# Performance work log

Hardware: AMD Instinct MI355X
Metric: run time of the kernel (lower is better)

## Reference

```python
import jax, jax.numpy as jnp
import numpy as np

N_NODES = 50000
N_EDGES = 800000
IN_DIM = 32
HID = 64
OUT_DIM = 4
HEADS = 4
LAYERS = 3
N_GRAPHS = 50
NEG_SLOPE = 0.2
BN_EPS = 1e-5


def setup_inputs() -> dict:
    key = jax.random.key(0)
    ks = jax.random.split(key, 20)
    x = jax.random.normal(ks[0], (N_NODES, IN_DIM), dtype=jnp.float32)
    edge_index = jax.random.randint(ks[1], (2, N_EDGES), 0, N_NODES, dtype=jnp.int64)
    batch = jnp.sort(jax.random.randint(ks[2], (N_NODES,), 0, N_GRAPHS, dtype=jnp.int64))
    s = 0.05
    inp = {
        "x": x,
        "edge_index": edge_index,
        "batch": batch,
        "in_W": jax.random.normal(ks[3], (IN_DIM, HID), jnp.float32) * s,
        "in_b": jnp.zeros((HID,), jnp.float32),
        "gat_W": jax.random.normal(ks[4], (LAYERS, HID, HEADS * HID), jnp.float32) * s,
        "att_src": jax.random.normal(ks[5], (LAYERS, HEADS, HID), jnp.float32) * s,
        "att_dst": jax.random.normal(ks[6], (LAYERS, HEADS, HID), jnp.float32) * s,
        "gat_b": jnp.zeros((LAYERS, HID), jnp.float32),
        "bn_g": jnp.ones((LAYERS, HID), jnp.float32),
        "bn_b": jnp.zeros((LAYERS, HID), jnp.float32),
        "bn_m": jnp.zeros((LAYERS, HID), jnp.float32),
        "bn_v": jnp.ones((LAYERS, HID), jnp.float32),
        "fc1_W": jax.random.normal(ks[7], (HID, HID), jnp.float32) * s,
        "fc1_b": jnp.zeros((HID,), jnp.float32),
        "fc2_W": jax.random.normal(ks[8], (HID, OUT_DIM), jnp.float32) * s,
        "fc2_b": jnp.zeros((OUT_DIM,), jnp.float32),
    }
    return inp


def _gat_layer(x, src, dst, W, a_src, a_dst, b):
    # x: [N, HID]; src/dst: [E'] (self-loops included)
    N = x.shape[0]
    xt = (x @ W).reshape(N, HEADS, HID)           # [N, H, C]
    sc_src = jnp.einsum("nhc,hc->nh", xt, a_src)  # [N, H]
    sc_dst = jnp.einsum("nhc,hc->nh", xt, a_dst)
    e = jax.nn.leaky_relu(sc_src[src] + sc_dst[dst], NEG_SLOPE)  # [E, H]
    # segment softmax over incoming edges of each dst node
    emax = jax.ops.segment_max(e, dst, num_segments=N)
    ex = jnp.exp(e - emax[dst])
    denom = jax.ops.segment_sum(ex, dst, num_segments=N)
    alpha = ex / (denom[dst] + 1e-16)             # [E, H]
    msg = xt[src] * alpha[:, :, None]             # [E, H, C]
    out = jax.ops.segment_sum(msg, dst, num_segments=N)  # [N, H, C]
    return out.mean(axis=1) + b                   # head-average (concat=False)


def reference(x, edge_index, batch, in_W, in_b, gat_W, att_src, att_dst, gat_b,
              bn_g, bn_b, bn_m, bn_v, fc1_W, fc1_b, fc2_W, fc2_b):
    N = x.shape[0]
    loops = jnp.arange(N, dtype=edge_index.dtype)
    src = jnp.concatenate([edge_index[0], loops])
    dst = jnp.concatenate([edge_index[1], loops])

    h = x @ in_W + in_b  # dropout: eval mode (identity)
    for i in range(LAYERS):
        identity = h
        h = _gat_layer(h, src, dst, gat_W[i], att_src[i], att_dst[i], gat_b[i])
        # BatchNorm1d in eval mode (running stats)
        h = (h - bn_m[i]) * jax.lax.rsqrt(bn_v[i] + BN_EPS) * bn_g[i] + bn_b[i]
        h = jax.nn.relu(h)
        h = h + identity

    # global mean pool over graphs
    sums = jax.ops.segment_sum(h, batch, num_segments=N_GRAPHS)
    cnt = jax.ops.segment_sum(jnp.ones((N,), h.dtype), batch, num_segments=N_GRAPHS)
    g = sums / jnp.maximum(cnt, 1.0)[:, None]     # [N_GRAPHS, HID]

    g = jax.nn.relu(g @ fc1_W + fc1_b)
    return g @ fc2_W + fc2_b                      # [N_GRAPHS, OUT_DIM]
```

## Files before the change

### kernel.cpp

```cpp
#include <hip/hip_runtime.h>
#include <hip/hip_fp16.h>
#include <math.h>

#define HID 64
#define HEADS 4
#define HC 256
#define IN_DIM 32
#define NEG 0.2f
#define BN_EPS 1e-5f
#define CAP 64

__device__ __forceinline__ int ld_idx(const int* __restrict__ p, int i, int f64) {
    return f64 ? p[(size_t)2 * i] : p[i];
}

__global__ void k_init(const int* __restrict__ ei, int* __restrict__ flag,
                       int* __restrict__ deg, float* __restrict__ gsum,
                       int N, int NG) {
    int i = blockIdx.x * blockDim.x + threadIdx.x;
    if (i == 0) {
        int z = 1;
#pragma unroll
        for (int k = 1; k < 64; k += 2) z &= (ei[k] == 0);
        *flag = z;
    }
    if (i < N) deg[i] = 0;
    if (i < NG) gsum[i] = 0.f;
}

template <typename IT>
__global__ void k_build(const int* __restrict__ ei, const int* __restrict__ flagp,
                        int* __restrict__ deg, IT* __restrict__ src_pad, int E) {
    int e = blockIdx.x * blockDim.x + threadIdx.x;
    if (e >= E) return;
    const int f = *flagp;
    int s = ld_idx(ei, e, f);
    int d = ld_idx(ei, E + e, f);
    int pos = atomicAdd(&deg[d], 1);
    if (pos < CAP) src_pad[(size_t)d * CAP + pos] = (IT)s;
}

__global__ void k_wtilde(const float* __restrict__ gat_W, const float* __restrict__ asrc,
                         const float* __restrict__ adst, float* __restrict__ wts,
                         float* __restrict__ wtd) {
    int l = blockIdx.x;
    int t = threadIdx.x;
    int hh = t >> 6, k = t & 63;
    const float* W = gat_W + (size_t)l * HID * HC + (size_t)k * HC + hh * HID;
    const float* as = asrc + (size_t)l * HEADS * HID + hh * HID;
    const float* ad = adst + (size_t)l * HEADS * HID + hh * HID;
    float s1 = 0.f, s2 = 0.f;
#pragma unroll
    for (int c = 0; c < HID; ++c) { s1 += W[c] * as[c]; s2 += W[c] * ad[c]; }
    wts[l * HC + hh * HID + k] = s1;
    wtd[l * HC + hh * HID + k] = s2;
}

__global__ __launch_bounds__(256) void k_input(
        const float* __restrict__ x, const float* __restrict__ W,
        const float* __restrict__ b, const float* __restrict__ wts0,
        const float* __restrict__ wtd0, float* __restrict__ h,
        __half* __restrict__ h16, float* __restrict__ ssrc,
        float* __restrict__ sdst, int N) {
    int w = threadIdx.x >> 6, lane = threadIdx.x & 63;
    int n = blockIdx.x * 4 + w;
    if (n >= N) return;
    float xv = x[(size_t)n * IN_DIM + (lane & 31)];
    float acc = b[lane];
#pragma unroll
    for (int k = 0; k < IN_DIM; ++k)
        acc += __shfl(xv, k, 64) * W[k * HID + lane];
    h[(size_t)n * HID + lane] = acc;
    h16[(size_t)n * HID + lane] = __float2half(acc);
    float p0 = acc * wts0[0 * HID + lane];
    float p1 = acc * wts0[1 * HID + lane];
    float p2 = acc * wts0[2 * HID + lane];
    float p3 = acc * wts0[3 * HID + lane];
    float q0 = acc * wtd0[0 * HID + lane];
    float q1 = acc * wtd0[1 * HID + lane];
    float q2 = acc * wtd0[2 * HID + lane];
    float q3 = acc * wtd0[3 * HID + lane];
#pragma unroll
    for (int m = 32; m >= 1; m >>= 1) {
        p0 += __shfl_xor(p0, m, 64); p1 += __shfl_xor(p1, m, 64);
        p2 += __shfl_xor(p2, m, 64); p3 += __shfl_xor(p3, m, 64);
        q0 += __shfl_xor(q0, m, 64); q1 += __shfl_xor(q1, m, 64);
        q2 += __shfl_xor(q2, m, 64); q3 += __shfl_xor(q3, m, 64);
    }
    if (lane == 0) {
        *(float4*)(ssrc + (size_t)n * HEADS) = make_float4(p0, p1, p2, p3);
        *(float4*)(sdst + (size_t)n * HEADS) = make_float4(q0, q1, q2, q3);
    }
}

template <typename IT>
__global__ __launch_bounds__(256) void k_gather(
        const int* __restrict__ deg, const IT* __restrict__ src_pad,
        const float* __restrict__ ssrc, const float* __restrict__ sdst,
        const __half* __restrict__ h16, __half* __restrict__ agg, int N) {
    int d = blockIdx.x * 4 + (threadIdx.x >> 6);
    if (d >= N) return;
    const int lane = threadIdx.x & 63;
    const int g = lane >> 4, l16 = lane & 15;
    const int dg = min(deg[d], CAP);
    const int se = (int)src_pad[(size_t)d * CAP + lane];
    const float4 sdd = *(const float4*)(sdst + (size_t)d * HEADS);
    float den0 = 0.f, den1 = 0.f, den2 = 0.f, den3 = 0.f;
    float a00=0.f,a01=0.f,a02=0.f,a03=0.f, a10=0.f,a11=0.f,a12=0.f,a13=0.f;
    float a20=0.f,a21=0.f,a22=0.f,a23=0.f, a30=0.f,a31=0.f,a32=0.f,a33=0.f;
    {
        float4 ssd = *(const float4*)(ssrc + (size_t)d * HEADS);
        uint2 hu = *(const uint2*)(h16 + (size_t)d * HID + l16 * 4);
        float2 f01 = __half22float2(*(__half2*)&hu.x);
        float2 f23 = __half22float2(*(__half2*)&hu.y);
        if (g == 0) {
            float v0 = ssd.x + sdd.x; v0 = v0 > 0.f ? v0 : NEG * v0;
            float v1 = ssd.y + sdd.y; v1 = v1 > 0.f ? v1 : NEG * v1;
            float v2 = ssd.z + sdd.z; v2 = v2 > 0.f ? v2 : NEG * v2;
            float v3 = ssd.w + sdd.w; v3 = v3 > 0.f ? v3 : NEG * v3;
            float e0 = __expf(v0), e1 = __expf(v1), e2 = __expf(v2), e3 = __expf(v3);
            den0 = e0; den1 = e1; den2 = e2; den3 = e3;
            a00 = e0*f01.x; a01 = e0*f01.y; a02 = e0*f23.x; a03 = e0*f23.y;
            a10 = e1*f01.x; a11 = e1*f01.y; a12 = e1*f23.x; a13 = e1*f23.y;
            a20 = e2*f01.x; a21 = e2*f01.y; a22 = e2*f23.x; a23 = e2*f23.y;
            a30 = e3*f01.x; a31 = e3*f01.y; a32 = e3*f23.x; a33 = e3*f23.y;
        }
    }
    for (int b = 0; b < dg; b += 4) {
        int idx = b + g;
        bool valid = idx < dg;
        int s = __shfl(se, idx, 64);
        s = valid ? s : d;
        float4 ss = *(const float4*)(ssrc + (size_t)s * HEADS);
        uint2 hu = *(const uint2*)(h16 + (size_t)s * HID + l16 * 4);
        float u0 = ss.x + sdd.x; u0 = u0 > 0.f ? u0 : NEG * u0;
        float u1 = ss.y + sdd.y; u1 = u1 > 0.f ? u1 : NEG * u1;
        float u2 = ss.z + sdd.z; u2 = u2 > 0.f ? u2 : NEG * u2;
        float u3 = ss.w + sdd.w; u3 = u3 > 0.f ? u3 : NEG * u3;
        float e0 = valid ? __expf(u0) : 0.f;
        float e1 = valid ? __expf(u1) : 0.f;
        float e2 = valid ? __expf(u2) : 0.f;
        float e3 = valid ? __expf(u3) : 0.f;
        float2 f01 = __half22float2(*(__half2*)&hu.x);
        float2 f23 = __half22float2(*(__half2*)&hu.y);
        den0 += e0; den1 += e1; den2 += e2; den3 += e3;
        a00 += e0*f01.x; a01 += e0*f01.y; a02 += e0*f23.x; a03 += e0*f23.y;
        a10 += e1*f01.x; a11 += e1*f01.y; a12 += e1*f23.x; a13 += e1*f23.y;
        a20 += e2*f01.x; a21 += e2*f01.y; a22 += e2*f23.x; a23 += e2*f23.y;
        a30 += e3*f01.x; a31 += e3*f01.y; a32 += e3*f23.x; a33 += e3*f23.y;
    }
#define FOLD(v) { v += __shfl_xor(v, 16, 64); v += __shfl_xor(v, 32, 64); }
    FOLD(den0) FOLD(den1) FOLD(den2) FOLD(den3)
    FOLD(a00) FOLD(a01) FOLD(a02) FOLD(a03)
    FOLD(a10) FOLD(a11) FOLD(a12) FOLD(a13)
    FOLD(a20) FOLD(a21) FOLD(a22) FOLD(a23)
    FOLD(a30) FOLD(a31) FOLD(a32) FOLD(a33)
#undef FOLD
    float iv, o0, o1, o2, o3;
    if (g == 0)      { iv = 0.25f / den0; o0 = a00; o1 = a01; o2 = a02; o3 = a03; }
    else if (g == 1) { iv = 0.25f / den1; o0 = a10; o1 = a11; o2 = a12; o3 = a13; }
    else if (g == 2) { iv = 0.25f / den2; o0 = a20; o1 = a21; o2 = a22; o3 = a23; }
    else             { iv = 0.25f / den3; o0 = a30; o1 = a31; o2 = a32; o3 = a33; }
    __half2 q01 = __floats2half2_rn(o0 * iv, o1 * iv);
    __half2 q23 = __floats2half2_rn(o2 * iv, o3 * iv);
    uint2 st;
    st.x = *(unsigned int*)&q01;
    st.y = *(unsigned int*)&q23;
    *(uint2*)(agg + ((size_t)d * HC + g * HID + l16 * 4)) = st;
}

#define PWB 16
__global__ __launch_bounds__(256) void k_postW(
        const __half* __restrict__ agg, const float* __restrict__ W,
        const float* __restrict__ gb, const float* __restrict__ bg,
        const float* __restrict__ bb, const float* __restrict__ bm,
        const float* __restrict__ bv, const float* __restrict__ wtsn,
        const float* __restrict__ wtdn, float* __restrict__ h,
        __half* __restrict__ h16, float* __restrict__ ssrc,
        float* __restrict__ sdst, int N) {
    __shared__ float sm[PWB * HC];
    const int t = threadIdx.x;
    const int n0 = blockIdx.x * PWB;
    {
        int j = t >> 4, c0 = (t & 15) * 16;
        float* dst = &sm[j * HC + c0];
        if (n0 + j < N) {
            const __half* src = agg + ((size_t)(n0 + j) * HC + c0);
            uint4 u0 = *(const uint4*)(src);
            uint4 u1 = *(const uint4*)(src + 8);
            const __half2* p0 = (const __half2*)&u0;
            const __half2* p1 = (const __half2*)&u1;
#pragma unroll
            for (int i = 0; i < 4; ++i) {
                float2 f = __half22float2(p0[i]);
                dst[2 * i] = f.x; dst[2 * i + 1] = f.y;
            }
#pragma unroll
            for (int i = 0; i < 4; ++i) {
                float2 f = __half22float2(p1[i]);
                dst[8 + 2 * i] = f.x; dst[8 + 2 * i + 1] = f.y;
            }
        } else {
#pragma unroll
            for (int i = 0; i < 16; ++i) dst[i] = 0.f;
        }
    }
    float wreg[HID];
#pragma unroll
    for (int k = 0; k < HID; ++k) wreg[k] = W[k * HC + t];
    __syncthreads();
    const int hh = t >> 6;
    float p[PWB];
#pragma unroll
    for (int j = 0; j < PWB; ++j) {
        const float* row = &sm[j * HC + hh * HID];
        float s = 0.f;
#pragma unroll
        for (int kk = 0; kk < HID / 4; ++kk) {
            float4 a = *(const float4*)(row + kk * 4);
            s += a.x * wreg[4 * kk + 0] + a.y * wreg[4 * kk + 1]
               + a.z * wreg[4 * kk + 2] + a.w * wreg[4 * kk + 3];
        }
        p[j] = s;
    }
    __syncthreads();
#pragma unroll
    for (int j = 0; j < PWB; ++j) sm[j * HC + t] = p[j];
    __syncthreads();
    {
        int j = t >> 4, c0 = (t & 15) * 4;
        int n = n0 + j;
        if (n < N) {
            float4 s0 = *(const float4*)&sm[j * HC + c0];
            float4 s1 = *(const float4*)&sm[j * HC + 64 + c0];
            float4 s2 = *(const float4*)&sm[j * HC + 128 + c0];
            float4 s3 = *(const float4*)&sm[j * HC + 192 + c0];
            float* hrow = h + (size_t)n * HID;
            float4 r = *(const float4*)(hrow + c0);
            float4 gb4 = *(const float4*)(gb + c0);
            float4 bg4 = *(const float4*)(bg + c0);
            float4 bb4 = *(const float4*)(bb + c0);
            float4 bm4 = *(const float4*)(bm + c0);
            float4 bv4 = *(const float4*)(bv + c0);
            float4 o;
            {
                float v = s0.x + s1.x + s2.x + s3.x + gb4.x;
                v = (v - bm4.x) * rsqrtf(bv4.x + BN_EPS) * bg4.x + bb4.x;
                o.x = fmaxf(v, 0.f) + r.x;
            }
            {
                float v = s0.y + s1.y + s2.y + s3.y + gb4.y;
                v = (v - bm4.y) * rsqrtf(bv4.y + BN_EPS) * bg4.y + bb4.y;
                o.y = fmaxf(v, 0.f) + r.y;
            }
            {
                float v = s0.z + s1.z + s2.z + s3.z + gb4.z;
                v = (v - bm4.z) * rsqrtf(bv4.z + BN_EPS) * bg4.z + bb4.z;
                o.z = fmaxf(v, 0.f) + r.z;
            }
            {
                float v = s0.w + s1.w + s2.w + s3.w + gb4.w;
                v = (v - bm4.w) * rsqrtf(bv4.w + BN_EPS) * bg4.w + bb4.w;
                o.w = fmaxf(v, 0.f) + r.w;
            }
            *(float4*)(hrow + c0) = o;
            __half2 ha = __floats2half2_rn(o.x, o.y);
            __half2 hb = __floats2half2_rn(o.z, o.w);
            uint2 hu;
            hu.x = *(unsigned int*)&ha;
            hu.y = *(unsigned int*)&hb;
            *(uint2*)(h16 + (size_t)n * HID + c0) = hu;
            if (wtsn) {
                float ps0 = 0.f, ps1 = 0.f, ps2 = 0.f, ps3 = 0.f;
                float pd0 = 0.f, pd1 = 0.f, pd2 = 0.f, pd3 = 0.f;
#pragma unroll
                for (int i = 0; i < 4; ++i) {
                    int c = c0 + i;
                    float ov = i == 0 ? o.x : i == 1 ? o.y : i == 2 ? o.z : o.w;
                    ps0 += ov * wtsn[0 * HID + c]; ps1 += ov * wtsn[1 * HID + c];
                    ps2 += ov * wtsn[2 * HID + c]; ps3 += ov * wtsn[3 * HID + c];
                    pd0 += ov * wtdn[0 * HID + c]; pd1 += ov * wtdn[1 * HID + c];
                    pd2 += ov * wtdn[2 * HID + c]; pd3 += ov * wtdn[3 * HID + c];
                }
#pragma unroll
                for (int m = 8; m >= 1; m >>= 1) {
                    ps0 += __shfl_xor(ps0, m, 64); ps1 += __shfl_xor(ps1, m, 64);
                    ps2 += __shfl_xor(ps2, m, 64); ps3 += __shfl_xor(ps3, m, 64);
                    pd0 += __shfl_xor(pd0, m, 64); pd1 += __shfl_xor(pd1, m, 64);
                    pd2 += __shfl_xor(pd2, m, 64); pd3 += __shfl_xor(pd3, m, 64);
                }
                if ((t & 15) == 0) {
                    *(float4*)(ssrc + (size_t)n * HEADS) = make_float4(ps0, ps1, ps2, ps3);
                    *(float4*)(sdst + (size_t)n * HEADS) = make_float4(pd0, pd1, pd2, pd3);
                }
            }
        }
    }
}

#define NPBK 64
__global__ void k_pool_sum(const float* __restrict__ h, const int* __restrict__ batch,
                           const int* __restrict__ flagp, float* __restrict__ gsum, int N) {
    const int f = *flagp;
    int c = threadIdx.x;
    int n0 = blockIdx.x * NPBK;
    int n1 = min(n0 + NPBK, N);
    if (n0 >= N) return;
    int cur = ld_idx(batch, n0, f);
    float s = 0.f;
    for (int n = n0; n < n1; ++n) {
        int g = ld_idx(batch, n, f);
        if (g != cur) {
            atomicAdd(&gsum[cur * HID + c], s);
            s = 0.f;
            cur = g;
        }
        s += h[(size_t)n * HID + c];
    }
    atomicAdd(&gsum[cur * HID + c], s);
}

__device__ __forceinline__ int lower_bound_i(const int* __restrict__ a, int n, int v, int f) {
    int lo = 0, hi = n;
    while (lo < hi) {
        int mid = (lo + hi) >> 1;
        if (ld_idx(a, mid, f) < v) lo = mid + 1; else hi = mid;
    }
    return lo;
}

__global__ void k_mlp(const float* __restrict__ gsum, const int* __restrict__ batch,
                      const int* __restrict__ flagp, int N,
                      const float* __restrict__ W1, const float* __restrict__ b1,
                      const float* __restrict__ W2, const float* __restrict__ b2,
                      float* __restrict__ out, int OUTD) {
    int gg = blockIdx.x, c = threadIdx.x;
    const int f = *flagp;
    int lo = lower_bound_i(batch, N, gg, f);
    int hi = lower_bound_i(batch, N, gg + 1, f);
    float cnt = (float)(hi - lo);
    __shared__ float gs[HID];
    __shared__ float s1[HID];
    gs[c] = gsum[gg * HID + c] / fmaxf(cnt, 1.f);
    __syncthreads();
    float acc = b1[c];
#pragma unroll
    for (int k = 0; k < HID; ++k) acc += gs[k] * W1[k * HID + c];
    s1[c] = fmaxf(acc, 0.f);
    __syncthreads();
    if (c < OUTD) {
        float o = b2[c];
#pragma unroll
        for (int k = 0; k < HID; ++k) o += s1[k] * W2[k * OUTD + c];
        out[gg * OUTD + c] = o;
    }
}

extern "C" void kernel_launch(void* const* d_in, const int* in_sizes, int n_in,
                              void* d_out, int out_size, void* d_ws, size_t ws_size,
                              hipStream_t stream) {
    const float* x       = (const float*)d_in[0];
    const int*   ei_raw  = (const int*)d_in[1];
    const int*   b_raw   = (const int*)d_in[2];
    const float* in_W    = (const float*)d_in[3];
    const float* in_b    = (const float*)d_in[4];
    const float* gat_W   = (const float*)d_in[5];
    const float* att_src = (const float*)d_in[6];
    const float* att_dst = (const float*)d_in[7];
    const float* gat_b   = (const float*)d_in[8];
    const float* bn_g    = (const float*)d_in[9];
    const float* bn_b    = (const float*)d_in[10];
    const float* bn_m    = (const float*)d_in[11];
    const float* bn_v    = (const float*)d_in[12];
    const float* fc1_W   = (const float*)d_in[13];
    const float* fc1_b   = (const float*)d_in[14];
    const float* fc2_W   = (const float*)d_in[15];
    const float* fc2_b   = (const float*)d_in[16];

    const int N = in_sizes[2];
    const int E = in_sizes[1] / 2;
    const int OUTD = 4;
    const int G = out_size / OUTD;

    float*  h    = (float*)d_ws;
    __half* h16  = (__half*)(h + (size_t)N * HID);
    __half* agg  = h16 + (size_t)N * HID;
    float*  ssrc = (float*)(agg + (size_t)N * HC);
    float*  sdst = ssrc + (size_t)N * HEADS;
    float*  wts  = sdst + (size_t)N * HEADS;
    float*  wtd  = wts + 3 * HC;
    float*  gsum = wtd + 3 * HC;
    int*    deg  = (int*)(gsum + (size_t)G * HID);
    unsigned short* src_pad = (unsigned short*)(deg + N);
    int*    flag = (int*)(src_pad + (size_t)N * CAP);

    k_init<<<(max(N, G * HID) + 255) / 256, 256, 0, stream>>>(
        ei_raw, flag, deg, gsum, N, G * HID);
    k_build<unsigned short><<<(E + 255) / 256, 256, 0, stream>>>(
        ei_raw, flag, deg, src_pad, E);
    k_wtilde<<<3, 256, 0, stream>>>(gat_W, att_src, att_dst, wts, wtd);
    k_input<<<(N + 3) / 4, 256, 0, stream>>>(x, in_W, in_b, wts, wtd, h, h16,
                                             ssrc, sdst, N);

    for (int l = 0; l < 3; ++l) {
        k_gather<unsigned short><<<(N + 3) / 4, 256, 0, stream>>>(
            deg, src_pad, ssrc, sdst, h16, agg, N);
        const float* wtsn = (l < 2) ? (wts + (l + 1) * HC) : nullptr;
        const float* wtdn = (l < 2) ? (wtd + (l + 1) * HC) : nullptr;
        k_postW<<<(N + PWB - 1) / PWB, 256, 0, stream>>>(
            agg, gat_W + (size_t)l * HID * HC,
            gat_b + (size_t)l * HID, bn_g + (size_t)l * HID, bn_b + (size_t)l * HID,
            bn_m + (size_t)l * HID, bn_v + (size_t)l * HID,
            wtsn, wtdn, h, h16, ssrc, sdst, N);
    }

    k_pool_sum<<<(N + NPBK - 1) / NPBK, HID, 0, stream>>>(h, b_raw, flag, gsum, N);
    k_mlp<<<G, HID, 0, stream>>>(gsum, b_raw, flag, N, fc1_W, fc1_b, fc2_W, fc2_b,
                                 (float*)d_out, OUTD);
}
```

Before: 375.1 us.

## Use MFMA for post-aggregation GEMM and bucket edges before CSR build

Replaces the scalar-FMA per-node projection in k_postW with fp16 MFMA 16x16x32 instructions, using a pre-transposed fp16 copy of the GAT weights and 64 rows per block. It also splits adjacency construction into two passes. Edges are first partitioned into 256-node destination buckets, reusing the agg buffer as scratch, and then each bucket is expanded into padded source lists, so the per-node degree atomics stay local. Weights are rounded to fp16, which reduces precision. Edge order within each node's list can now differ, and any bucket that overflows its capacity silently drops edges.

```diff
diff --git a/kernel.cpp b/kernel.cpp
--- a/kernel.cpp
+++ b/kernel.cpp
@@ -10,13 +10,17 @@
 #define BN_EPS 1e-5f
 #define CAP 64
 
+typedef _Float16 f16;
+typedef _Float16 f16x8 __attribute__((ext_vector_type(8)));
+typedef float f32x4 __attribute__((ext_vector_type(4)));
+
 __device__ __forceinline__ int ld_idx(const int* __restrict__ p, int i, int f64) {
     return f64 ? p[(size_t)2 * i] : p[i];
 }
 
 __global__ void k_init(const int* __restrict__ ei, int* __restrict__ flag,
-                       int* __restrict__ deg, float* __restrict__ gsum,
-                       int N, int NG) {
+                       int* __restrict__ deg, int* __restrict__ cursor,
+                       float* __restrict__ gsum, int N, int NG) {
     int i = blockIdx.x * blockDim.x + threadIdx.x;
     if (i == 0) {
         int z = 1;
@@ -25,19 +29,36 @@
         *flag = z;
     }
     if (i < N) deg[i] = 0;
+    if (i < 256) cursor[i] = 0;
     if (i < NG) gsum[i] = 0.f;
 }
 
-template <typename IT>
-__global__ void k_build(const int* __restrict__ ei, const int* __restrict__ flagp,
-                        int* __restrict__ deg, IT* __restrict__ src_pad, int E) {
+__global__ void k_part(const int* __restrict__ ei, const int* __restrict__ flagp,
+                       int* __restrict__ cursor, unsigned int* __restrict__ edge_tmp,
+                       int E, int capb) {
     int e = blockIdx.x * blockDim.x + threadIdx.x;
     if (e >= E) return;
     const int f = *flagp;
-    int s = ld_idx(ei, e, f);
-    int d = ld_idx(ei, E + e, f);
-    int pos = atomicAdd(&deg[d], 1);
-    if (pos < CAP) src_pad[(size_t)d * CAP + pos] = (IT)s;
+    unsigned int s = (unsigned int)ld_idx(ei, e, f);
+    unsigned int d = (unsigned int)ld_idx(ei, E + e, f);
+    int b = d >> 8;
+    int pos = atomicAdd(&cursor[b], 1);
+    if (pos < capb)
+        edge_tmp[(size_t)b * capb + pos] = ((d & 255u) << 16) | s;
+}
+
+__global__ void k_bucket(const unsigned int* __restrict__ edge_tmp,
+                         const int* __restrict__ cursor, int* __restrict__ deg,
+                         unsigned short* __restrict__ src_pad, int capb, int N) {
+    int b = blockIdx.x;
+    int cnt = min(cursor[b], capb);
+    for (int i = threadIdx.x; i < cnt; i += blockDim.x) {
+        unsigned int rec = edge_tmp[(size_t)b * capb + i];
+        int d = (b << 8) + (int)(rec >> 16);
+        int s = (int)(rec & 0xffffu);
+        int pos = atomicAdd(&deg[d], 1);
+        if (pos < CAP) src_pad[(size_t)d * CAP + pos] = (unsigned short)s;
+    }
 }
 
 __global__ void k_wtilde(const float* __restrict__ gat_W, const float* __restrict__ asrc,
@@ -54,6 +75,17 @@
     for (int c = 0; c < HID; ++c) { s1 += W[c] * as[c]; s2 += W[c] * ad[c]; }
     wts[l * HC + hh * HID + k] = s1;
     wtd[l * HC + hh * HID + k] = s2;
+}
+
+__global__ void k_prepB(const float* __restrict__ gat_W, __half* __restrict__ BT) {
+    int l = blockIdx.x;
+    int t = threadIdx.x;
+    int c = t & 63, jg = t >> 6;
+    const float* W = gat_W + (size_t)l * HID * HC;
+    __half* o = BT + (size_t)l * HID * HC + (size_t)c * HC + jg * 64;
+#pragma unroll
+    for (int jj = 0; jj < 64; ++jj)
+        o[jj] = __float2half(W[(size_t)jj * HC + jg * 64 + c]);
 }
 
 __global__ __launch_bounds__(256) void k_input(
@@ -93,9 +125,8 @@
     }
 }
 
-template <typename IT>
 __global__ __launch_bounds__(256) void k_gather(
-        const int* __restrict__ deg, const IT* __restrict__ src_pad,
+        const int* __restrict__ deg, const unsigned short* __restrict__ src_pad,
         const float* __restrict__ ssrc, const float* __restrict__ sdst,
         const __half* __restrict__ h16, __half* __restrict__ agg, int N) {
     int d = blockIdx.x * 4 + (threadIdx.x >> 6);
@@ -169,127 +200,108 @@
     *(uint2*)(agg + ((size_t)d * HC + g * HID + l16 * 4)) = st;
 }
 
-#define PWB 16
 __global__ __launch_bounds__(256) void k_postW(
-        const __half* __restrict__ agg, const float* __restrict__ W,
+        const __half* __restrict__ agg, const __half* __restrict__ BT,
         const float* __restrict__ gb, const float* __restrict__ bg,
         const float* __restrict__ bb, const float* __restrict__ bm,
         const float* __restrict__ bv, const float* __restrict__ wtsn,
         const float* __restrict__ wtdn, float* __restrict__ h,
         __half* __restrict__ h16, float* __restrict__ ssrc,
         float* __restrict__ sdst, int N) {
-    __shared__ float sm[PWB * HC];
+    __shared__ float lds[64][68];
     const int t = threadIdx.x;
-    const int n0 = blockIdx.x * PWB;
-    {
-        int j = t >> 4, c0 = (t & 15) * 16;
-        float* dst = &sm[j * HC + c0];
-        if (n0 + j < N) {
-            const __half* src = agg + ((size_t)(n0 + j) * HC + c0);
-            uint4 u0 = *(const uint4*)(src);
-            uint4 u1 = *(const uint4*)(src + 8);
-            const __half2* p0 = (const __half2*)&u0;
-            const __half2* p1 = (const __half2*)&u1;
-#pragma unroll
-            for (int i = 0; i < 4; ++i) {
-                float2 f = __half22float2(p0[i]);
-                dst[2 * i] = f.x; dst[2 * i + 1] = f.y;
-            }
-#pragma unroll
-            for (int i = 0; i < 4; ++i) {
-                float2 f = __half22float2(p1[i]);
-                dst[8 + 2 * i] = f.x; dst[8 + 2 * i + 1] = f.y;
-            }
-        } else {
-#pragma unroll
-            for (int i = 0; i < 16; ++i) dst[i] = 0.f;
-        }
-    }
-    float wreg[HID];
-#pragma unroll
-    for (int k = 0; k < HID; ++k) wreg[k] = W[k * HC + t];
-    __syncthreads();
-    const int hh = t >> 6;
-    float p[PWB];
-#pragma unroll
-    for (int j = 0; j < PWB; ++j) {
-        const float* row = &sm[j * HC + hh * HID];
-        float s = 0.f;
-#pragma unroll
-        for (int kk = 0; kk < HID / 4; ++kk) {
-            float4 a = *(const float4*)(row + kk * 4);
-            s += a.x * wreg[4 * kk + 0] + a.y * wreg[4 * kk + 1]
-               + a.z * wreg[4 * kk + 2] + a.w * wreg[4 * kk + 3];
-        }
-        p[j] = s;
-    }
-    __syncthreads();
-#pragma unroll
-    for (int j = 0; j < PWB; ++j) sm[j * HC + t] = p[j];
+    const int w = t >> 6, l = t & 63;
+    const int l16 = l & 15, lk = l >> 4;
+    const f16* BTf = (const f16*)BT;
+    const f16* af = (const f16*)agg;
+    f16x8 bf[8][4];
+#pragma unroll
+    for (int ks = 0; ks < 8; ++ks)
+#pragma unroll
+        for (int nt = 0; nt < 4; ++nt)
+            bf[ks][nt] = *(const f16x8*)(BTf + (size_t)(nt * 16 + l16) * HC + ks * 32 + lk * 8);
+    int row = blockIdx.x * 64 + w * 16 + l16;
+    int rowc = min(row, N - 1);
+    f32x4 acc[4];
+#pragma unroll
+    for (int nt = 0; nt < 4; ++nt) acc[nt] = (f32x4){0.f, 0.f, 0.f, 0.f};
+#pragma unroll
+    for (int ks = 0; ks < 8; ++ks) {
+        f16x8 a = *(const f16x8*)(af + (size_t)rowc * HC + ks * 32 + lk * 8);
+#pragma unroll
+        for (int nt = 0; nt < 4; ++nt)
+            acc[nt] = __builtin_amdgcn_mfma_f32_16x16x32_f16(a, bf[ks][nt], acc[nt], 0, 0, 0);
+    }
+#pragma unroll
+    for (int nt = 0; nt < 4; ++nt)
+#pragma unroll
+        for (int r = 0; r < 4; ++r)
+            lds[w * 16 + lk * 4 + r][nt * 16 + l16] = acc[nt][r];
     __syncthreads();
     {
-        int j = t >> 4, c0 = (t & 15) * 4;
-        int n = n0 + j;
+        int j = t >> 2, q = t & 3;
+        int n = blockIdx.x * 64 + j;
         if (n < N) {
-            float4 s0 = *(const float4*)&sm[j * HC + c0];
-            float4 s1 = *(const float4*)&sm[j * HC + 64 + c0];
-            float4 s2 = *(const float4*)&sm[j * HC + 128 + c0];
-            float4 s3 = *(const float4*)&sm[j * HC + 192 + c0];
+            int c0 = q * 16;
+            float o[16];
             float* hrow = h + (size_t)n * HID;
-            float4 r = *(const float4*)(hrow + c0);
-            float4 gb4 = *(const float4*)(gb + c0);
-            float4 bg4 = *(const float4*)(bg + c0);
-            float4 bb4 = *(const float4*)(bb + c0);
-            float4 bm4 = *(const float4*)(bm + c0);
-            float4 bv4 = *(const float4*)(bv + c0);
-            float4 o;
-            {
-                float v = s0.x + s1.x + s2.x + s3.x + gb4.x;
-                v = (v - bm4.x) * rsqrtf(bv4.x + BN_EPS) * bg4.x + bb4.x;
-                o.x = fmaxf(v, 0.f) + r.x;
+#pragma unroll
+            for (int i4 = 0; i4 < 4; ++i4) {
+                int c = c0 + i4 * 4;
+                float4 sv = *(const float4*)&lds[j][c];
+                float4 r4 = *(const float4*)(hrow + c);
+                float4 gb4 = *(const float4*)(gb + c);
+                float4 bg4 = *(const float4*)(bg + c);
+                float4 bb4 = *(const float4*)(bb + c);
+                float4 bm4 = *(const float4*)(bm + c);
+                float4 bv4 = *(const float4*)(bv + c);
+                float4 ov;
+                float v;
+                v = sv.x + gb4.x; v = (v - bm4.x) * rsqrtf(bv4.x + BN_EPS) * bg4.x + bb4.x;
+                ov.x = fmaxf(v, 0.f) + r4.x;
+                v = sv.y + gb4.y; v = (v - bm4.y) * rsqrtf(bv4.y + BN_EPS) * bg4.y + bb4.y;
+                ov.y = fmaxf(v, 0.f) + r4.y;
+                v = sv.z + gb4.z; v = (v - bm4.z) * rsqrtf(bv4.z + BN_EPS) * bg4.z + bb4.z;
+                ov.z = fmaxf(v, 0.f) + r4.z;
+                v = sv.w + gb4.w; v = (v - bm4.w) * rsqrtf(bv4.w + BN_EPS) * bg4.w + bb4.w;
+                ov.w = fmaxf(v, 0.f) + r4.w;
+                *(float4*)(hrow + c) = ov;
+                o[i4 * 4 + 0] = ov.x; o[i4 * 4 + 1] = ov.y;
+                o[i4 * 4 + 2] = ov.z; o[i4 * 4 + 3] = ov.w;
             }
             {
-                float v = s0.y + s1.y + s2.y + s3.y + gb4.y;
-                v = (v - bm4.y) * rsqrtf(bv4.y + BN_EPS) * bg4.y + bb4.y;
-                o.y = fmaxf(v, 0.f) + r.y;
+                __half2 hp[8];
+#pragma unroll
+                for (int i = 0; i < 8; ++i)
+                    hp[i] = __floats2half2_rn(o[2 * i], o[2 * i + 1]);
+                uint4 u0, u1;
+                u0.x = *(unsigned*)&hp[0]; u0.y = *(unsigned*)&hp[1];
+                u0.z = *(unsigned*)&hp[2]; u0.w = *(unsigned*)&hp[3];
+                u1.x = *(unsigned*)&hp[4]; u1.y = *(unsigned*)&hp[5];
+                u1.z = *(unsigned*)&hp[6]; u1.w = *(unsigned*)&hp[7];
+                *(uint4*)(h16 + (size_t)n * HID + c0) = u0;
+                *(uint4*)(h16 + (size_t)n * HID + c0 + 8) = u1;
             }
-            {
-                float v = s0.z + s1.z + s2.z + s3.z + gb4.z;
-                v = (v - bm4.z) * rsqrtf(bv4.z + BN_EPS) * bg4.z + bb4.z;
-                o.z = fmaxf(v, 0.f) + r.z;
-            }
-            {
-                float v = s0.w + s1.w + s2.w + s3.w + gb4.w;
-                v = (v - bm4.w) * rsqrtf(bv4.w + BN_EPS) * bg4.w + bb4.w;
-                o.w = fmaxf(v, 0.f) + r.w;
-            }
-            *(float4*)(hrow + c0) = o;
-            __half2 ha = __floats2half2_rn(o.x, o.y);
-            __half2 hb = __floats2half2_rn(o.z, o.w);
-            uint2 hu;
-            hu.x = *(unsigned int*)&ha;
-            hu.y = *(unsigned int*)&hb;
-            *(uint2*)(h16 + (size_t)n * HID + c0) = hu;
             if (wtsn) {
                 float ps0 = 0.f, ps1 = 0.f, ps2 = 0.f, ps3 = 0.f;
                 float pd0 = 0.f, pd1 = 0.f, pd2 = 0.f, pd3 = 0.f;
 #pragma unroll
-                for (int i = 0; i < 4; ++i) {
+                for (int i = 0; i < 16; ++i) {
                     int c = c0 + i;
-                    float ov = i == 0 ? o.x : i == 1 ? o.y : i == 2 ? o.z : o.w;
+                    float ov = o[i];
                     ps0 += ov * wtsn[0 * HID + c]; ps1 += ov * wtsn[1 * HID + c];
                     ps2 += ov * wtsn[2 * HID + c]; ps3 += ov * wtsn[3 * HID + c];
                     pd0 += ov * wtdn[0 * HID + c]; pd1 += ov * wtdn[1 * HID + c];
                     pd2 += ov * wtdn[2 * HID + c]; pd3 += ov * wtdn[3 * HID + c];
                 }
 #pragma unroll
-                for (int m = 8; m >= 1; m >>= 1) {
+                for (int m = 2; m >= 1; m >>= 1) {
                     ps0 += __shfl_xor(ps0, m, 64); ps1 += __shfl_xor(ps1, m, 64);
                     ps2 += __shfl_xor(ps2, m, 64); ps3 += __shfl_xor(ps3, m, 64);
                     pd0 += __shfl_xor(pd0, m, 64); pd1 += __shfl_xor(pd1, m, 64);
                     pd2 += __shfl_xor(pd2, m, 64); pd3 += __shfl_xor(pd3, m, 64);
                 }
-                if ((t & 15) == 0) {
+                if (q == 0) {
                     *(float4*)(ssrc + (size_t)n * HEADS) = make_float4(ps0, ps1, ps2, ps3);
                     *(float4*)(sdst + (size_t)n * HEADS) = make_float4(pd0, pd1, pd2, pd3);
                 }
@@ -381,34 +393,43 @@
     const int E = in_sizes[1] / 2;
     const int OUTD = 4;
     const int G = out_size / OUTD;
+    const int nbuck = (N + 255) >> 8;
+    int capb = ((2 * E / nbuck) + 1023) & ~1023;
 
     float*  h    = (float*)d_ws;
     __half* h16  = (__half*)(h + (size_t)N * HID);
     __half* agg  = h16 + (size_t)N * HID;
+    unsigned int* edge_tmp = (unsigned int*)agg;
     float*  ssrc = (float*)(agg + (size_t)N * HC);
     float*  sdst = ssrc + (size_t)N * HEADS;
     float*  wts  = sdst + (size_t)N * HEADS;
     float*  wtd  = wts + 3 * HC;
-    float*  gsum = wtd + 3 * HC;
+    __half* BT   = (__half*)(wtd + 3 * HC);
+    float*  gsum = (float*)(BT + 3 * HID * HC);
     int*    deg  = (int*)(gsum + (size_t)G * HID);
     unsigned short* src_pad = (unsigned short*)(deg + N);
-    int*    flag = (int*)(src_pad + (size_t)N * CAP);
+    int*    cursor = (int*)(src_pad + (size_t)N * CAP);
+    int*    flag = cursor + 256;
+
+    if ((size_t)nbuck * capb * 4 > (size_t)N * HC * 2)
+        capb = (int)(((size_t)N * HC * 2) / (4 * (size_t)nbuck)) & ~63;
 
     k_init<<<(max(N, G * HID) + 255) / 256, 256, 0, stream>>>(
-        ei_raw, flag, deg, gsum, N, G * HID);
-    k_build<unsigned short><<<(E + 255) / 256, 256, 0, stream>>>(
-        ei_raw, flag, deg, src_pad, E);
+        ei_raw, flag, deg, cursor, gsum, N, G * HID);
+    k_part<<<(E + 255) / 256, 256, 0, stream>>>(ei_raw, flag, cursor, edge_tmp, E, capb);
+    k_bucket<<<nbuck, 256, 0, stream>>>(edge_tmp, cursor, deg, src_pad, capb, N);
     k_wtilde<<<3, 256, 0, stream>>>(gat_W, att_src, att_dst, wts, wtd);
+    k_prepB<<<3, 256, 0, stream>>>(gat_W, BT);
     k_input<<<(N + 3) / 4, 256, 0, stream>>>(x, in_W, in_b, wts, wtd, h, h16,
                                              ssrc, sdst, N);
 
     for (int l = 0; l < 3; ++l) {
-        k_gather<unsigned short><<<(N + 3) / 4, 256, 0, stream>>>(
+        k_gather<<<(N + 3) / 4, 256, 0, stream>>>(
             deg, src_pad, ssrc, sdst, h16, agg, N);
         const float* wtsn = (l < 2) ? (wts + (l + 1) * HC) : nullptr;
         const float* wtdn = (l < 2) ? (wtd + (l + 1) * HC) : nullptr;
-        k_postW<<<(N + PWB - 1) / PWB, 256, 0, stream>>>(
-            agg, gat_W + (size_t)l * HID * HC,
+        k_postW<<<(N + 63) / 64, 256, 0, stream>>>(
+            agg, BT + (size_t)l * HID * HC,
             gat_b + (size_t)l * HID, bn_g + (size_t)l * HID, bn_b + (size_t)l * HID,
             bn_m + (size_t)l * HID, bn_v + (size_t)l * HID,
             wtsn, wtdn, h, h16, ssrc, sdst, N);
```

Result: slower. 765.5 us (+104.0%).
